# Performance work log

Measured on AMD Instinct MI355X. Metric: run time of the kernel, lower is better.

The kernel has to match this reference:

```python
import jax, jax.numpy as jnp
import numpy as np

D_MODEL = 1024
D_STATE = 16
D_CONV = 4
EXPAND = 2
HEADDIM = 8
D_INNER = EXPAND * D_MODEL            # 2048
NHEADS = D_INNER // HEADDIM           # 256
CONV_DIM = D_INNER + 2 * D_STATE      # 2080 (ngroups=1)
D_IN_PROJ = 2 * D_INNER + 2 * D_STATE + NHEADS  # 4384
B_SZ, SEQ = 4, 2048
EPS = 1e-5


def setup_inputs() -> dict:
    key = jax.random.key(0)
    ks = jax.random.split(key, 8)
    return {
        "x": jax.random.normal(ks[0], (B_SZ, SEQ, D_MODEL), jnp.float32),
        "ln_w": jnp.ones((D_MODEL,), jnp.float32),
        "ln_b": jnp.zeros((D_MODEL,), jnp.float32),
        "W_in": jax.random.normal(ks[1], (D_MODEL, D_IN_PROJ), jnp.float32) * 0.02,
        "conv_w": jax.random.normal(ks[2], (D_CONV, 1, CONV_DIM), jnp.float32) * 0.2,
        "conv_b": jnp.zeros((CONV_DIM,), jnp.float32),
        "A_log": jnp.log(jax.random.uniform(ks[3], (NHEADS,), jnp.float32, 1.0, 16.0)),
        "Dp": jnp.ones((NHEADS,), jnp.float32) + 0.1 * jax.random.normal(ks[4], (NHEADS,), jnp.float32),
        "dt_bias": 0.5 * jax.random.normal(ks[5], (NHEADS,), jnp.float32),
        "rms_w": jnp.ones((D_INNER,), jnp.float32),
        "W_out": jax.random.normal(ks[6], (D_INNER, D_MODEL), jnp.float32) * 0.02,
    }


def _mamba_block(x, ln_w, ln_b, W_in, conv_w, conv_b, A_log, Dp, dt_bias, rms_w, W_out):
    B, L, _ = x.shape
    # pre-norm LayerNorm
    mu = jnp.mean(x, axis=-1, keepdims=True)
    var = jnp.mean((x - mu) ** 2, axis=-1, keepdims=True)
    xn = (x - mu) * jax.lax.rsqrt(var + EPS) * ln_w + ln_b

    # in_proj -> z, xBC, dt
    u = xn @ W_in                                    # (B, L, 4384)
    z = u[..., :D_INNER]
    xBC = u[..., D_INNER:D_INNER + CONV_DIM]
    dt = jax.nn.softplus(u[..., -NHEADS:] + dt_bias)  # (B, L, NHEADS)

    # causal depthwise conv1d + SiLU
    xp = jnp.pad(xBC, ((0, 0), (D_CONV - 1, 0), (0, 0)))
    xBC = jax.lax.conv_general_dilated(
        xp, conv_w, window_strides=(1,), padding="VALID",
        dimension_numbers=("NWC", "WIO", "NWC"), feature_group_count=CONV_DIM)
    xBC = jax.nn.silu(xBC + conv_b)

    xs = xBC[..., :D_INNER].reshape(B, L, NHEADS, HEADDIM)   # SSM input
    Bm = xBC[..., D_INNER:D_INNER + D_STATE]                  # (B, L, N)
    Cm = xBC[..., D_INNER + D_STATE:]                          # (B, L, N)

    A = -jnp.exp(A_log)                                       # (NHEADS,)

    def step(h, inp):
        # h: (B, H, P, N)
        x_t, B_t, C_t, dt_t = inp
        dA = jnp.exp(dt_t * A)                                 # (B, H)
        h = h * dA[..., None, None] + jnp.einsum("bh,bhp,bn->bhpn", dt_t, x_t, B_t)
        y = jnp.einsum("bhpn,bn->bhp", h, C_t)
        return h, y

    h0 = jnp.zeros((B, NHEADS, HEADDIM, D_STATE), x.dtype)
    _, ys = jax.lax.scan(step, h0, (xs.swapaxes(0, 1), Bm.swapaxes(0, 1),
                                     Cm.swapaxes(0, 1), dt.swapaxes(0, 1)))
    y = ys.swapaxes(0, 1) + Dp[None, None, :, None] * xs       # (B, L, H, P)
    y = y.reshape(B, L, D_INNER)

    # gated RMSNorm: rmsnorm(y * silu(z)) * weight
    g = y * jax.nn.silu(z)
    g = g * jax.lax.rsqrt(jnp.mean(g * g, axis=-1, keepdims=True) + EPS) * rms_w

    return x + g @ W_out


def reference(x, ln_w, ln_b, W_in, conv_w, conv_b, A_log, Dp, dt_bias, rms_w, W_out):
    return _mamba_block(x, ln_w, ln_b, W_in, conv_w, conv_b, A_log, Dp, dt_bias, rms_w, W_out)
```

## Files before the change

### kernel.cpp

```cpp
#include <hip/hip_runtime.h>

typedef __bf16 bf16;
typedef __attribute__((ext_vector_type(8))) __bf16 bf16x8;
typedef __attribute__((ext_vector_type(4))) float f32x4;

#define B_SZ 4
#define SEQ 2048
#define DM 1024
#define DIN 2048
#define NH 256
#define DSTATE 16
#define CONVD 2080
#define DPROJ 4384
#define NPAD1 4608
#define MROWS 8192
#define NC 32
#define LC 64
#define UROWB 8768

__device__ __forceinline__ void gload_lds16(const void* g, void* l) {
  __builtin_amdgcn_global_load_lds(
      (__attribute__((address_space(1))) void*)g,
      (__attribute__((address_space(3))) void*)l, 16, 0, 0);
}

template <int N>
__device__ __forceinline__ void vm_wait() {
  asm volatile("s_waitcnt vmcnt(%0)" ::"n"(N) : "memory");
}
__device__ __forceinline__ void bar() { asm volatile("s_barrier" ::: "memory"); }
__device__ __forceinline__ void lgkm0() {
  asm volatile("s_waitcnt lgkmcnt(0)" ::: "memory");
}

__global__ void transpose_cvt(const float* __restrict__ W, bf16* __restrict__ WT,
                              int K, int N, int Npad, const float* __restrict__ rw) {
  __shared__ float tile[32][33];
  int k0 = blockIdx.x * 32, n0 = blockIdx.y * 32;
  int tx = threadIdx.x, ty = threadIdx.y;
#pragma unroll
  for (int j = 0; j < 4; j++) {
    int k = k0 + ty + 8 * j, n = n0 + tx;
    float v = (k < K && n < N) ? W[(size_t)k * N + n] : 0.f;
    if (rw && k < K) v *= rw[k];
    tile[ty + 8 * j][tx] = v;
  }
  __syncthreads();
#pragma unroll
  for (int j = 0; j < 4; j++) {
    int n = n0 + ty + 8 * j, k = k0 + tx;
    if (n < Npad && k < K) WT[(size_t)n * K + k] = (bf16)tile[tx][ty + 8 * j];
  }
}

__global__ __launch_bounds__(256) void ln_kernel(const float* __restrict__ x,
                                                 const float* __restrict__ lw,
                                                 const float* __restrict__ lb,
                                                 bf16* __restrict__ xn) {
  int row = blockIdx.x;
  int t = threadIdx.x;
  f32x4 v4 = ((const f32x4*)(x + (size_t)row * DM))[t];
  float v0 = v4[0], v1 = v4[1], v2 = v4[2], v3 = v4[3];
  float s = v0 + v1 + v2 + v3;
  float s2 = v0 * v0 + v1 * v1 + v2 * v2 + v3 * v3;
#pragma unroll
  for (int off = 32; off > 0; off >>= 1) {
    s += __shfl_down(s, off);
    s2 += __shfl_down(s2, off);
  }
  __shared__ float ps[8];
  int wave = t >> 6, lane = t & 63;
  if (lane == 0) { ps[wave] = s; ps[4 + wave] = s2; }
  __syncthreads();
  s = ps[0] + ps[1] + ps[2] + ps[3];
  s2 = ps[4] + ps[5] + ps[6] + ps[7];
  float mean = s * (1.f / DM);
  float var = s2 * (1.f / DM) - mean * mean;
  float rstd = rsqrtf(var + 1e-5f);
  f32x4 wv = ((const f32x4*)lw)[t];
  f32x4 bv = ((const f32x4*)lb)[t];
  bf16 o[4];
  o[0] = (bf16)((v0 - mean) * rstd * wv[0] + bv[0]);
  o[1] = (bf16)((v1 - mean) * rstd * wv[1] + bv[1]);
  o[2] = (bf16)((v2 - mean) * rstd * wv[2] + bv[2]);
  o[3] = (bf16)((v3 - mean) * rstd * wv[3] + bv[3]);
  bf16* dst = xn + (size_t)row * DM + t * 4;
  dst[0] = o[0]; dst[1] = o[1]; dst[2] = o[2]; dst[3] = o[3];
}

__global__ __launch_bounds__(512, 2) void gemm1_8p(const bf16* __restrict__ A,
                                                   const bf16* __restrict__ BT,
                                                   bf16* __restrict__ C) {
  __shared__ char lds[139264];
  int bid = blockIdx.x;
  int xcd = bid & 7;
  int l = bid >> 3;
  int bm = xcd * 4 + ((l >> 3) & 3);
  int bn = (l >> 5) * 8 + (l & 7);
  int m0 = bm * 256, n0 = bn * 192;
  int t = threadIdx.x, lane = t & 63, wave = t >> 6;
  int wm = wave >> 2, wn = wave & 3;
  int lr16 = lane & 15, kq = lane >> 4;
  int ts0 = kq ^ (lr16 & 7);
  int ts1 = (4 + kq) ^ (lr16 & 7);
  int sw = (lane & 7) ^ (lane >> 3);
  int l8 = lane >> 3;
  const char* Ab = (const char*)A;
  const char* Bb = (const char*)BT;

  auto stA = [&](int kt) {
    char* slot = lds + (kt & 1) * 32768;
    size_t ko = (size_t)kt * 128 + sw * 16;
#pragma unroll
    for (int g = 0; g < 4; g++) {
      int c = wave * 4 + g;
      gload_lds16(Ab + (size_t)(m0 + c * 8 + l8) * 2048 + ko, slot + c * 1024);
    }
  };
  auto stB = [&](int kt) {
    char* slot = lds + 65536 + (kt % 3) * 24576;
    size_t ko = (size_t)kt * 128 + sw * 16;
#pragma unroll
    for (int g = 0; g < 3; g++) {
      int c = wave * 3 + g;
      gload_lds16(Bb + (size_t)(n0 + c * 8 + l8) * 2048 + ko, slot + c * 1024);
    }
  };

  f32x4 acc[8][3] = {};
  bf16x8 a_[4][2], b_[3][2];

  stA(0); stB(0); stA(1); stB(1);
  vm_wait<7>();
  bar();
#pragma unroll 1
  for (int kt = 0; kt < 16; kt++) {
    {
      const char* sa = lds + (kt & 1) * 32768;
      const char* sb = lds + 65536 + (kt % 3) * 24576;
#pragma unroll
      for (int mi = 0; mi < 4; mi++) {
        int lrow = wm * 128 + mi * 16 + lr16;
        a_[mi][0] = *(const bf16x8*)(sa + lrow * 128 + ts0 * 16);
        a_[mi][1] = *(const bf16x8*)(sa + lrow * 128 + ts1 * 16);
      }
#pragma unroll
      for (int ni = 0; ni < 3; ni++) {
        int lrow = wn * 48 + ni * 16 + lr16;
        b_[ni][0] = *(const bf16x8*)(sb + lrow * 128 + ts0 * 16);
        b_[ni][1] = *(const bf16x8*)(sb + lrow * 128 + ts1 * 16);
      }
      if (kt >= 1 && kt < 15) stA(kt + 1);
      if (kt < 14) stB(kt + 2);
      bar();
      lgkm0();
      __builtin_amdgcn_s_setprio(1);
#pragma unroll
      for (int mi = 0; mi < 4; mi++)
#pragma unroll
        for (int ni = 0; ni < 3; ni++) {
          acc[mi][ni] = __builtin_amdgcn_mfma_f32_16x16x32_bf16(a_[mi][0], b_[ni][0], acc[mi][ni], 0, 0, 0);
          acc[mi][ni] = __builtin_amdgcn_mfma_f32_16x16x32_bf16(a_[mi][1], b_[ni][1], acc[mi][ni], 0, 0, 0);
        }
      __builtin_amdgcn_s_setprio(0);
      bar();
    }
    {
      const char* sa = lds + (kt & 1) * 32768;
#pragma unroll
      for (int mi = 0; mi < 4; mi++) {
        int lrow = wm * 128 + 64 + mi * 16 + lr16;
        a_[mi][0] = *(const bf16x8*)(sa + lrow * 128 + ts0 * 16);
        a_[mi][1] = *(const bf16x8*)(sa + lrow * 128 + ts1 * 16);
      }
      if (kt <= 13) vm_wait<3>();
      else if (kt == 14) vm_wait<0>();
      bar();
      lgkm0();
      __builtin_amdgcn_s_setprio(1);
#pragma unroll
      for (int mi = 0; mi < 4; mi++)
#pragma unroll
        for (int ni = 0; ni < 3; ni++) {
          acc[4 + mi][ni] = __builtin_amdgcn_mfma_f32_16x16x32_bf16(a_[mi][0], b_[ni][0], acc[4 + mi][ni], 0, 0, 0);
          acc[4 + mi][ni] = __builtin_amdgcn_mfma_f32_16x16x32_bf16(a_[mi][1], b_[ni][1], acc[4 + mi][ni], 0, 0, 0);
        }
      __builtin_amdgcn_s_setprio(0);
      bar();
    }
  }
#pragma unroll
  for (int fr = 0; fr < 8; fr++)
#pragma unroll
    for (int ni = 0; ni < 3; ni++) {
      int row = m0 + wm * 128 + fr * 16 + kq * 4;
      int col = n0 + wn * 48 + ni * 16 + lr16;
      f32x4 v = acc[fr][ni];
      if (col < 4384) {
#pragma unroll
        for (int r = 0; r < 4; r++)
          C[(size_t)(row + r) * DPROJ + col] = (bf16)v[r];
      }
    }
}

__global__ __launch_bounds__(512, 2) void gemm2_8p(const bf16* __restrict__ A,
                                                   const bf16* __restrict__ BT,
                                                   float* __restrict__ C,
                                                   const float* __restrict__ Xres) {
  __shared__ char lds[147456];
  int bid = blockIdx.x;
  int swz = (bid & 7) * 32 + (bid >> 3);
  int bm = swz >> 2, bn = swz & 3;
  int m0 = bm * 128, n0 = bn * 256;
  int t = threadIdx.x, lane = t & 63, wave = t >> 6;
  int wm = wave >> 2, wn = wave & 3;
  int lr16 = lane & 15, kq = lane >> 4;
  int ts0 = kq ^ (lr16 & 7);
  int ts1 = (4 + kq) ^ (lr16 & 7);
  int sw = (lane & 7) ^ (lane >> 3);
  int l8 = lane >> 3;
  const char* Ab = (const char*)A;
  const char* Bb = (const char*)BT;

  auto stA = [&](int kt) {
    char* slot = lds + (kt % 3) * 16384;
    size_t ko = (size_t)kt * 128 + sw * 16;
#pragma unroll
    for (int g = 0; g < 2; g++) {
      int c = wave * 2 + g;
      gload_lds16(Ab + (size_t)(m0 + c * 8 + l8) * 4096 + ko, slot + c * 1024);
    }
  };
  auto stB = [&](int kt) {
    char* slot = lds + 49152 + (kt % 3) * 32768;
    size_t ko = (size_t)kt * 128 + sw * 16;
#pragma unroll
    for (int g = 0; g < 4; g++) {
      int c = wave * 4 + g;
      gload_lds16(Bb + (size_t)(n0 + c * 8 + l8) * 4096 + ko, slot + c * 1024);
    }
  };

  f32x4 acc[4][4] = {};
  bf16x8 a_[4][2], b_[2][2];
  float s2a[4] = {0.f, 0.f, 0.f, 0.f};

  stA(0); stB(0); stA(1); stB(1);
  vm_wait<6>();
  bar();
#pragma unroll 1
  for (int kt = 0; kt < 32; kt++) {
    const char* sa = lds + (kt % 3) * 16384;
    const char* sb = lds + 49152 + (kt % 3) * 32768;
    {
#pragma unroll
      for (int mi = 0; mi < 4; mi++) {
        int lrow = wm * 64 + mi * 16 + lr16;
        a_[mi][0] = *(const bf16x8*)(sa + lrow * 128 + ts0 * 16);
        a_[mi][1] = *(const bf16x8*)(sa + lrow * 128 + ts1 * 16);
      }
#pragma unroll
      for (int ni = 0; ni < 2; ni++) {
        int lrow = wn * 64 + ni * 16 + lr16;
        b_[ni][0] = *(const bf16x8*)(sb + lrow * 128 + ts0 * 16);
        b_[ni][1] = *(const bf16x8*)(sb + lrow * 128 + ts1 * 16);
      }
      if (kt + 2 < 32) { stA(kt + 2); stB(kt + 2); }
      bar();
      lgkm0();
      __builtin_amdgcn_s_setprio(1);
#pragma unroll
      for (int mi = 0; mi < 4; mi++)
#pragma unroll
        for (int ni = 0; ni < 2; ni++) {
          acc[mi][ni] = __builtin_amdgcn_mfma_f32_16x16x32_bf16(a_[mi][0], b_[ni][0], acc[mi][ni], 0, 0, 0);
          acc[mi][ni] = __builtin_amdgcn_mfma_f32_16x16x32_bf16(a_[mi][1], b_[ni][1], acc[mi][ni], 0, 0, 0);
        }
      __builtin_amdgcn_s_setprio(0);
      bar();
    }
    {
#pragma unroll
      for (int ni = 0; ni < 2; ni++) {
        int lrow = wn * 64 + (2 + ni) * 16 + lr16;
        b_[ni][0] = *(const bf16x8*)(sb + lrow * 128 + ts0 * 16);
        b_[ni][1] = *(const bf16x8*)(sb + lrow * 128 + ts1 * 16);
      }
      if (kt <= 29) vm_wait<6>();
      else if (kt == 30) vm_wait<0>();
      bar();
      lgkm0();
      __builtin_amdgcn_s_setprio(1);
#pragma unroll
      for (int mi = 0; mi < 4; mi++)
#pragma unroll
        for (int ni = 0; ni < 2; ni++) {
          acc[mi][2 + ni] = __builtin_amdgcn_mfma_f32_16x16x32_bf16(a_[mi][0], b_[ni][0], acc[mi][2 + ni], 0, 0, 0);
          acc[mi][2 + ni] = __builtin_amdgcn_mfma_f32_16x16x32_bf16(a_[mi][1], b_[ni][1], acc[mi][2 + ni], 0, 0, 0);
        }
      __builtin_amdgcn_s_setprio(0);
#pragma unroll
      for (int mi = 0; mi < 4; mi++) {
        float s = 0.f;
#pragma unroll
        for (int si = 0; si < 2; si++)
#pragma unroll
          for (int e = 0; e < 8; e++) {
            float v = (float)a_[mi][si][e];
            s += v * v;
          }
        s2a[mi] += s;
      }
      bar();
    }
  }
#pragma unroll
  for (int mi = 0; mi < 4; mi++) {
    s2a[mi] += __shfl_xor(s2a[mi], 16);
    s2a[mi] += __shfl_xor(s2a[mi], 32);
  }
  float* scaleL = (float*)lds;
  if (wn == 0 && kq == 0) {
#pragma unroll
    for (int mi = 0; mi < 4; mi++)
      scaleL[wm * 64 + mi * 16 + lr16] = rsqrtf(s2a[mi] * (1.f / 2048.f) + 1e-5f);
  }
  __syncthreads();
#pragma unroll
  for (int mi = 0; mi < 4; mi++)
#pragma unroll
    for (int ni = 0; ni < 4; ni++) {
      int rloc = wm * 64 + mi * 16 + kq * 4;
      int col = n0 + wn * 64 + ni * 16 + lr16;
      f32x4 v = acc[mi][ni];
#pragma unroll
      for (int r = 0; r < 4; r++) {
        float sc = scaleL[rloc + r];
        size_t o = (size_t)(m0 + rloc + r) * DM + col;
        C[o] = Xres[o] + sc * v[r];
      }
    }
}

__global__ __launch_bounds__(256) void conv_prep3(const bf16* __restrict__ u,
                                                  const float* __restrict__ cw,
                                                  const float* __restrict__ cb,
                                                  const float* __restrict__ dt_bias,
                                                  bf16* __restrict__ xs,
                                                  float* __restrict__ BC,
                                                  float* __restrict__ dtf) {
  const int JPR = 292;
  int idx = blockIdx.x * 256 + threadIdx.x;
  if (idx >= MROWS * JPR) return;
  int row = idx / JPR;
  int j = idx - row * JPR;
  int t = row & (SEQ - 1);
  if (j < 260) {
    int c0 = j * 8;
    float acc[8];
#pragma unroll
    for (int i = 0; i < 8; i++) acc[i] = cb[c0 + i];
    const bf16* ub = u + (size_t)row * DPROJ + DIN + c0;
#pragma unroll
    for (int tap = 0; tap < 4; tap++) {
      int tt = t - 3 + tap;
      if (tt >= 0) {
        bf16x8 uv = *(const bf16x8*)(ub + (ptrdiff_t)(tap - 3) * DPROJ);
        const float* wv = cw + tap * CONVD + c0;
#pragma unroll
        for (int i = 0; i < 8; i++) acc[i] += wv[i] * (float)uv[i];
      }
    }
    if (c0 < DIN) {
      bf16x8 o;
#pragma unroll
      for (int i = 0; i < 8; i++) {
        float sv = acc[i] / (1.f + __expf(-acc[i]));
        o[i] = (bf16)sv;
      }
      *(bf16x8*)(xs + (size_t)row * DIN + c0) = o;
    } else {
      float* bc = BC + (size_t)row * 32 + (c0 - DIN);
#pragma unroll
      for (int i = 0; i < 8; i++) bc[i] = acc[i] / (1.f + __expf(-acc[i]));
    }
  } else {
    int h0 = (j - 260) * 8;
    bf16x8 uv = *(const bf16x8*)(u + (size_t)row * DPROJ + (DPROJ - NH) + h0);
    float* dst = dtf + (size_t)row * NH + h0;
#pragma unroll
    for (int i = 0; i < 8; i++) {
      float xv = (float)uv[i] + dt_bias[h0 + i];
      dst[i] = (xv > 20.f) ? xv : log1pf(__expf(xv));
    }
  }
}

__global__ __launch_bounds__(64) void scan_p1(const bf16* __restrict__ xs,
                                              const float* __restrict__ BC,
                                              const float* __restrict__ dtf,
                                              const float* __restrict__ A_log,
                                              bf16* __restrict__ uscr) {
  int c = blockIdx.x & 31, hg = (blockIdx.x >> 5) & 31, b = blockIdx.x >> 10;
  int lane = threadIdx.x, hh = lane >> 3;
  int h = hg * 8 + hh;
  float A = -__expf(A_log[h]);
  float st[16];
#pragma unroll
  for (int n = 0; n < 16; n++) st[n] = 0.f;
  float pcum = 1.f;
  size_t rb = (size_t)b * SEQ + (size_t)c * LC;
#pragma unroll 2
  for (int t = 0; t < LC; t++) {
    size_t row = rb + t;
    const float* bcrow = BC + row * 32;
    float dtv = dtf[row * NH + h];
    float x = (float)xs[row * DIN + hg * 64 + lane];
    float dA = __expf(dtv * A);
    pcum *= dA;
    float w = dtv * x;
#pragma unroll
    for (int n = 0; n < 16; n++) st[n] = st[n] * dA + w * bcrow[n];
  }
  char* slot = (char*)uscr + (size_t)blockIdx.x * UROWB + 4096;
  float* S = (float*)slot;
#pragma unroll
  for (int n = 0; n < 16; n++) S[lane * 16 + n] = st[n];
  if ((lane & 7) == 0) ((float*)(slot + 4096))[hh] = pcum;
}

__global__ __launch_bounds__(64) void scan_p2(bf16* __restrict__ uscr) {
  int bh = blockIdx.x;
  int lane = threadIdx.x, hh = lane >> 3;
  float H[16];
#pragma unroll
  for (int n = 0; n < 16; n++) H[n] = 0.f;
  char* base = (char*)uscr + (size_t)bh * NC * UROWB + 4096;
  float sN[16], PN;
  {
    float* S = (float*)base;
#pragma unroll
    for (int n = 0; n < 16; n++) sN[n] = S[lane * 16 + n];
    PN = ((const float*)(base + 4096))[hh];
  }
  for (int c = 0; c < NC; c++) {
    float sC[16], PC = PN;
#pragma unroll
    for (int n = 0; n < 16; n++) sC[n] = sN[n];
    if (c + 1 < NC) {
      char* slot = base + (size_t)(c + 1) * UROWB;
      float* S = (float*)slot;
#pragma unroll
      for (int n = 0; n < 16; n++) sN[n] = S[lane * 16 + n];
      PN = ((const float*)(slot + 4096))[hh];
    }
    float* S0 = (float*)(base + (size_t)c * UROWB);
#pragma unroll
    for (int n = 0; n < 16; n++) {
      float hn = H[n];
      S0[lane * 16 + n] = hn;
      H[n] = PC * hn + sC[n];
    }
  }
}

__global__ __launch_bounds__(64) void scan_p3(const bf16* __restrict__ xs,
                                              const float* __restrict__ BC,
                                              const float* __restrict__ dtf,
                                              const float* __restrict__ A_log,
                                              const float* __restrict__ Dp,
                                              const bf16* __restrict__ u,
                                              bf16* __restrict__ g) {
  int c = blockIdx.x & 31, hg = (blockIdx.x >> 5) & 31, b = blockIdx.x >> 10;
  int lane = threadIdx.x, hh = lane >> 3;
  int h = hg * 8 + hh;
  float A = -__expf(A_log[h]);
  float D = Dp[h];
  const char* slot = (const char*)u + (size_t)blockIdx.x * UROWB + 4096;
  float st[16];
#pragma unroll
  for (int n = 0; n < 16; n++) st[n] = ((const float*)slot)[lane * 16 + n];
  size_t rb = (size_t)b * SEQ + (size_t)c * LC;
#pragma unroll 2
  for (int t = 0; t < LC; t++) {
    size_t row = rb + t;
    const float* bcrow = BC + row * 32;
    float dtv = dtf[row * NH + h];
    float x = (float)xs[row * DIN + hg * 64 + lane];
    float dA = __expf(dtv * A);
    float w = dtv * x;
    float yv = 0.f;
#pragma unroll
    for (int n = 0; n < 16; n++) {
      st[n] = st[n] * dA + w * bcrow[n];
      yv += st[n] * bcrow[16 + n];
    }
    float z = (float)u[row * DPROJ + hg * 64 + lane];
    float gg = (yv + D * x) * (z / (1.f + __expf(-z)));
    g[row * DIN + hg * 64 + lane] = (bf16)gg;
  }
}

extern "C" void kernel_launch(void* const* d_in, const int* in_sizes, int n_in,
                              void* d_out, int out_size, void* d_ws, size_t ws_size,
                              hipStream_t stream) {
  const float* x = (const float*)d_in[0];
  const float* lnw = (const float*)d_in[1];
  const float* lnb = (const float*)d_in[2];
  const float* Win = (const float*)d_in[3];
  const float* cw = (const float*)d_in[4];
  const float* cb = (const float*)d_in[5];
  const float* Alog = (const float*)d_in[6];
  const float* Dpv = (const float*)d_in[7];
  const float* dtb = (const float*)d_in[8];
  const float* rmsw = (const float*)d_in[9];
  const float* Wout = (const float*)d_in[10];
  float* out = (float*)d_out;

  char* ws = (char*)d_ws;
  bf16* u = (bf16*)(ws + 0);
  bf16* xnb = (bf16*)(ws + 71827456);
  bf16* WinT = (bf16*)(ws + 88604672);
  bf16* gb = (bf16*)(ws + 71827456);
  bf16* xsb = (bf16*)(ws + 105381888);
  float* BC = (float*)(ws + 138936320);
  float* dtf = (float*)(ws + 139984896);
  bf16* WoutT = (bf16*)(ws + 148373504);

  transpose_cvt<<<dim3(32, 144), dim3(32, 8), 0, stream>>>(Win, WinT, 1024, DPROJ, NPAD1, nullptr);
  transpose_cvt<<<dim3(64, 32), dim3(32, 8), 0, stream>>>(Wout, WoutT, DIN, DM, DM, rmsw);
  ln_kernel<<<MROWS, 256, 0, stream>>>(x, lnw, lnb, xnb);
  gemm1_8p<<<768, 512, 0, stream>>>(xnb, WinT, u);
  conv_prep3<<<(MROWS * 292) / 256, 256, 0, stream>>>(u, cw, cb, dtb, xsb, BC, dtf);
  scan_p1<<<4096, 64, 0, stream>>>(xsb, BC, dtf, Alog, u);
  scan_p2<<<128, 64, 0, stream>>>(u);
  scan_p3<<<4096, 64, 0, stream>>>(xsb, BC, dtf, Alog, Dpv, u, gb);
  gemm2_8p<<<256, 512, 0, stream>>>(gb, WoutT, out, x);
}
```

Baseline: 292.3 us.

## Fuse depthwise conv, SiLU and softplus into scan passes, drop xs/dt buffers

The conv+SiLU on the x channels and the softplus on dt now run inline in scan_p1 and scan_p3, each reading the raw projection output u directly. A rolling 3-tap window is kept in registers, with a halo loaded from the previous chunk. Only the small B/C conv stays as a separate kernel, and the chunk-state scratch moves to a dedicated float buffer. This removes the write and re-read of the xs and dtf intermediates, but the conv and softplus are now computed twice, once in each scan pass, and the strided u reads may coalesce less well.

```diff
diff --git a/kernel.cpp b/kernel.cpp
--- a/kernel.cpp
+++ b/kernel.cpp
@@ -16,7 +16,7 @@
 #define MROWS 8192
 #define NC 32
 #define LC 64
-#define UROWB 8768
+#define SLOTF 1056
 
 __device__ __forceinline__ void gload_lds16(const void* g, void* l) {
   __builtin_amdgcn_global_load_lds(
@@ -343,119 +343,105 @@
     }
 }
 
-__global__ __launch_bounds__(256) void conv_prep3(const bf16* __restrict__ u,
-                                                  const float* __restrict__ cw,
-                                                  const float* __restrict__ cb,
-                                                  const float* __restrict__ dt_bias,
-                                                  bf16* __restrict__ xs,
-                                                  float* __restrict__ BC,
-                                                  float* __restrict__ dtf) {
-  const int JPR = 292;
+__global__ __launch_bounds__(256) void conv_bc(const bf16* __restrict__ u,
+                                               const float* __restrict__ cw,
+                                               const float* __restrict__ cb,
+                                               float* __restrict__ BC) {
   int idx = blockIdx.x * 256 + threadIdx.x;
-  if (idx >= MROWS * JPR) return;
-  int row = idx / JPR;
-  int j = idx - row * JPR;
+  if (idx >= MROWS * 4) return;
+  int row = idx >> 2, j = idx & 3;
   int t = row & (SEQ - 1);
-  if (j < 260) {
-    int c0 = j * 8;
-    float acc[8];
-#pragma unroll
-    for (int i = 0; i < 8; i++) acc[i] = cb[c0 + i];
-    const bf16* ub = u + (size_t)row * DPROJ + DIN + c0;
-#pragma unroll
-    for (int tap = 0; tap < 4; tap++) {
-      int tt = t - 3 + tap;
-      if (tt >= 0) {
-        bf16x8 uv = *(const bf16x8*)(ub + (ptrdiff_t)(tap - 3) * DPROJ);
-        const float* wv = cw + tap * CONVD + c0;
-#pragma unroll
-        for (int i = 0; i < 8; i++) acc[i] += wv[i] * (float)uv[i];
-      }
-    }
-    if (c0 < DIN) {
-      bf16x8 o;
-#pragma unroll
-      for (int i = 0; i < 8; i++) {
-        float sv = acc[i] / (1.f + __expf(-acc[i]));
-        o[i] = (bf16)sv;
-      }
-      *(bf16x8*)(xs + (size_t)row * DIN + c0) = o;
-    } else {
-      float* bc = BC + (size_t)row * 32 + (c0 - DIN);
-#pragma unroll
-      for (int i = 0; i < 8; i++) bc[i] = acc[i] / (1.f + __expf(-acc[i]));
-    }
-  } else {
-    int h0 = (j - 260) * 8;
-    bf16x8 uv = *(const bf16x8*)(u + (size_t)row * DPROJ + (DPROJ - NH) + h0);
-    float* dst = dtf + (size_t)row * NH + h0;
-#pragma unroll
-    for (int i = 0; i < 8; i++) {
-      float xv = (float)uv[i] + dt_bias[h0 + i];
-      dst[i] = (xv > 20.f) ? xv : log1pf(__expf(xv));
-    }
-  }
-}
-
-__global__ __launch_bounds__(64) void scan_p1(const bf16* __restrict__ xs,
+  int cc = 2048 + j * 8;
+  float acc[8];
+#pragma unroll
+  for (int i = 0; i < 8; i++) acc[i] = cb[cc + i];
+  const bf16* ub = u + (size_t)row * DPROJ + DIN + cc;
+#pragma unroll
+  for (int tap = 0; tap < 4; tap++) {
+    if (t - 3 + tap >= 0) {
+      bf16x8 uv = *(const bf16x8*)(ub + (ptrdiff_t)(tap - 3) * DPROJ);
+      const float* wv = cw + tap * CONVD + cc;
+#pragma unroll
+      for (int i = 0; i < 8; i++) acc[i] += wv[i] * (float)uv[i];
+    }
+  }
+  float* bc = BC + (size_t)row * 32 + j * 8;
+#pragma unroll
+  for (int i = 0; i < 8; i++) bc[i] = acc[i] / (1.f + __expf(-acc[i]));
+}
+
+__global__ __launch_bounds__(64) void scan_p1(const bf16* __restrict__ u,
                                               const float* __restrict__ BC,
-                                              const float* __restrict__ dtf,
                                               const float* __restrict__ A_log,
-                                              bf16* __restrict__ uscr) {
+                                              const float* __restrict__ cw,
+                                              const float* __restrict__ cb,
+                                              const float* __restrict__ dt_bias,
+                                              float* __restrict__ scr) {
   int c = blockIdx.x & 31, hg = (blockIdx.x >> 5) & 31, b = blockIdx.x >> 10;
   int lane = threadIdx.x, hh = lane >> 3;
   int h = hg * 8 + hh;
+  int ch = hg * 64 + lane;
   float A = -__expf(A_log[h]);
+  float dtbh = dt_bias[h];
+  float w0 = cw[ch], w1 = cw[CONVD + ch], w2 = cw[2 * CONVD + ch], w3 = cw[3 * CONVD + ch];
+  float cbc = cb[ch];
+  size_t rb = (size_t)b * SEQ + (size_t)c * LC;
+  const bf16* ux = u + rb * DPROJ + DIN + ch;
+  const bf16* ud = u + rb * DPROJ + 4128 + h;
+  float um3 = 0.f, um2 = 0.f, um1 = 0.f;
+  if (c > 0) {
+    um3 = (float)ux[-3 * (ptrdiff_t)DPROJ];
+    um2 = (float)ux[-2 * (ptrdiff_t)DPROJ];
+    um1 = (float)ux[-1 * (ptrdiff_t)DPROJ];
+  }
   float st[16];
 #pragma unroll
   for (int n = 0; n < 16; n++) st[n] = 0.f;
   float pcum = 1.f;
-  size_t rb = (size_t)b * SEQ + (size_t)c * LC;
-#pragma unroll 2
   for (int t = 0; t < LC; t++) {
-    size_t row = rb + t;
-    const float* bcrow = BC + row * 32;
-    float dtv = dtf[row * NH + h];
-    float x = (float)xs[row * DIN + hg * 64 + lane];
+    float uc = (float)ux[(size_t)t * DPROJ];
+    float ca = cbc + w0 * um3 + w1 * um2 + w2 * um1 + w3 * uc;
+    um3 = um2; um2 = um1; um1 = uc;
+    float x = ca / (1.f + __expf(-ca));
+    float dv = (float)ud[(size_t)t * DPROJ] + dtbh;
+    float dtv = (dv > 20.f) ? dv : log1pf(__expf(dv));
+    const float* bcrow = BC + (rb + t) * 32;
     float dA = __expf(dtv * A);
     pcum *= dA;
     float w = dtv * x;
 #pragma unroll
     for (int n = 0; n < 16; n++) st[n] = st[n] * dA + w * bcrow[n];
   }
-  char* slot = (char*)uscr + (size_t)blockIdx.x * UROWB + 4096;
-  float* S = (float*)slot;
+  float* S = scr + (size_t)blockIdx.x * SLOTF;
 #pragma unroll
   for (int n = 0; n < 16; n++) S[lane * 16 + n] = st[n];
-  if ((lane & 7) == 0) ((float*)(slot + 4096))[hh] = pcum;
-}
-
-__global__ __launch_bounds__(64) void scan_p2(bf16* __restrict__ uscr) {
+  if ((lane & 7) == 0) S[1024 + hh] = pcum;
+}
+
+__global__ __launch_bounds__(64) void scan_p2(float* __restrict__ scr) {
   int bh = blockIdx.x;
   int lane = threadIdx.x, hh = lane >> 3;
   float H[16];
 #pragma unroll
   for (int n = 0; n < 16; n++) H[n] = 0.f;
-  char* base = (char*)uscr + (size_t)bh * NC * UROWB + 4096;
+  float* base = scr + (size_t)(bh * 32) * SLOTF;
   float sN[16], PN;
   {
-    float* S = (float*)base;
-#pragma unroll
-    for (int n = 0; n < 16; n++) sN[n] = S[lane * 16 + n];
-    PN = ((const float*)(base + 4096))[hh];
+#pragma unroll
+    for (int n = 0; n < 16; n++) sN[n] = base[lane * 16 + n];
+    PN = base[1024 + hh];
   }
   for (int c = 0; c < NC; c++) {
     float sC[16], PC = PN;
 #pragma unroll
     for (int n = 0; n < 16; n++) sC[n] = sN[n];
     if (c + 1 < NC) {
-      char* slot = base + (size_t)(c + 1) * UROWB;
-      float* S = (float*)slot;
+      float* S = base + (size_t)(c + 1) * SLOTF;
 #pragma unroll
       for (int n = 0; n < 16; n++) sN[n] = S[lane * 16 + n];
-      PN = ((const float*)(slot + 4096))[hh];
-    }
-    float* S0 = (float*)(base + (size_t)c * UROWB);
+      PN = S[1024 + hh];
+    }
+    float* S0 = base + (size_t)c * SLOTF;
 #pragma unroll
     for (int n = 0; n < 16; n++) {
       float hn = H[n];
@@ -465,29 +451,46 @@
   }
 }
 
-__global__ __launch_bounds__(64) void scan_p3(const bf16* __restrict__ xs,
+__global__ __launch_bounds__(64) void scan_p3(const bf16* __restrict__ u,
                                               const float* __restrict__ BC,
-                                              const float* __restrict__ dtf,
                                               const float* __restrict__ A_log,
                                               const float* __restrict__ Dp,
-                                              const bf16* __restrict__ u,
+                                              const float* __restrict__ cw,
+                                              const float* __restrict__ cb,
+                                              const float* __restrict__ dt_bias,
+                                              const float* __restrict__ scr,
                                               bf16* __restrict__ g) {
   int c = blockIdx.x & 31, hg = (blockIdx.x >> 5) & 31, b = blockIdx.x >> 10;
   int lane = threadIdx.x, hh = lane >> 3;
   int h = hg * 8 + hh;
+  int ch = hg * 64 + lane;
   float A = -__expf(A_log[h]);
   float D = Dp[h];
-  const char* slot = (const char*)u + (size_t)blockIdx.x * UROWB + 4096;
+  float dtbh = dt_bias[h];
+  float w0 = cw[ch], w1 = cw[CONVD + ch], w2 = cw[2 * CONVD + ch], w3 = cw[3 * CONVD + ch];
+  float cbc = cb[ch];
+  size_t rb = (size_t)b * SEQ + (size_t)c * LC;
+  const bf16* ux = u + rb * DPROJ + DIN + ch;
+  const bf16* ud = u + rb * DPROJ + 4128 + h;
+  const bf16* uz = u + rb * DPROJ + ch;
+  float um3 = 0.f, um2 = 0.f, um1 = 0.f;
+  if (c > 0) {
+    um3 = (float)ux[-3 * (ptrdiff_t)DPROJ];
+    um2 = (float)ux[-2 * (ptrdiff_t)DPROJ];
+    um1 = (float)ux[-1 * (ptrdiff_t)DPROJ];
+  }
+  const float* S = scr + (size_t)blockIdx.x * SLOTF;
   float st[16];
 #pragma unroll
-  for (int n = 0; n < 16; n++) st[n] = ((const float*)slot)[lane * 16 + n];
-  size_t rb = (size_t)b * SEQ + (size_t)c * LC;
-#pragma unroll 2
+  for (int n = 0; n < 16; n++) st[n] = S[lane * 16 + n];
   for (int t = 0; t < LC; t++) {
-    size_t row = rb + t;
-    const float* bcrow = BC + row * 32;
-    float dtv = dtf[row * NH + h];
-    float x = (float)xs[row * DIN + hg * 64 + lane];
+    float uc = (float)ux[(size_t)t * DPROJ];
+    float ca = cbc + w0 * um3 + w1 * um2 + w2 * um1 + w3 * uc;
+    um3 = um2; um2 = um1; um1 = uc;
+    float x = ca / (1.f + __expf(-ca));
+    float dv = (float)ud[(size_t)t * DPROJ] + dtbh;
+    float dtv = (dv > 20.f) ? dv : log1pf(__expf(dv));
+    const float* bcrow = BC + (rb + t) * 32;
     float dA = __expf(dtv * A);
     float w = dtv * x;
     float yv = 0.f;
@@ -496,9 +499,9 @@
       st[n] = st[n] * dA + w * bcrow[n];
       yv += st[n] * bcrow[16 + n];
     }
-    float z = (float)u[row * DPROJ + hg * 64 + lane];
+    float z = (float)uz[(size_t)t * DPROJ];
     float gg = (yv + D * x) * (z / (1.f + __expf(-z)));
-    g[row * DIN + hg * 64 + lane] = (bf16)gg;
+    g[(rb + t) * DIN + ch] = (bf16)gg;
   }
 }
 
@@ -523,18 +526,17 @@
   bf16* xnb = (bf16*)(ws + 71827456);
   bf16* WinT = (bf16*)(ws + 88604672);
   bf16* gb = (bf16*)(ws + 71827456);
-  bf16* xsb = (bf16*)(ws + 105381888);
+  float* scr = (float*)(ws + 105381888);
   float* BC = (float*)(ws + 138936320);
-  float* dtf = (float*)(ws + 139984896);
   bf16* WoutT = (bf16*)(ws + 148373504);
 
   transpose_cvt<<<dim3(32, 144), dim3(32, 8), 0, stream>>>(Win, WinT, 1024, DPROJ, NPAD1, nullptr);
   transpose_cvt<<<dim3(64, 32), dim3(32, 8), 0, stream>>>(Wout, WoutT, DIN, DM, DM, rmsw);
   ln_kernel<<<MROWS, 256, 0, stream>>>(x, lnw, lnb, xnb);
   gemm1_8p<<<768, 512, 0, stream>>>(xnb, WinT, u);
-  conv_prep3<<<(MROWS * 292) / 256, 256, 0, stream>>>(u, cw, cb, dtb, xsb, BC, dtf);
-  scan_p1<<<4096, 64, 0, stream>>>(xsb, BC, dtf, Alog, u);
-  scan_p2<<<128, 64, 0, stream>>>(u);
-  scan_p3<<<4096, 64, 0, stream>>>(xsb, BC, dtf, Alog, Dpv, u, gb);
+  conv_bc<<<(MROWS * 4) / 256, 256, 0, stream>>>(u, cw, cb, BC);
+  scan_p1<<<4096, 64, 0, stream>>>(u, BC, Alog, cw, cb, dtb, scr);
+  scan_p2<<<128, 64, 0, stream>>>(scr);
+  scan_p3<<<4096, 64, 0, stream>>>(u, BC, Alog, Dpv, cw, cb, dtb, scr, gb);
   gemm2_8p<<<256, 512, 0, stream>>>(gb, WoutT, out, x);
 }
```

Result: slower. 376.7 us (+28.9%).
